# Optimization experiments

Hardware: AMD Instinct MI355X
Metric: run time of the kernel (lower is better)

Reference implementation:

```python
import jax, jax.numpy as jnp
import numpy as np

N, E, B, L, D, H = 50000, 800000, 64, 32, 256, 256


def setup_inputs() -> dict:
    key = jax.random.key(0)
    ks = jax.random.split(key, 20)
    s = 0.05
    inp = {
        'x': jax.random.normal(ks[0], (N, D), jnp.float32),
        'edge_index': jax.random.randint(ks[1], (2, E), 0, N),
        'batch': jnp.sort(jax.random.randint(ks[2], (N,), 0, B)),
        'paths': jax.random.randint(ks[3], (B, L), 0, N),
        # SAGEConv1: lin_l (aggregated neighbors, with bias) + lin_r (root, no bias)
        'w1l': jax.random.normal(ks[4], (D, H), jnp.float32) * s,
        'b1l': jnp.zeros((H,), jnp.float32),
        'w1r': jax.random.normal(ks[5], (D, H), jnp.float32) * s,
        # SAGEConv2
        'w2l': jax.random.normal(ks[6], (H, H), jnp.float32) * s,
        'b2l': jnp.zeros((H,), jnp.float32),
        'w2r': jax.random.normal(ks[7], (H, H), jnp.float32) * s,
        # LSTM (gate order i,f,g,o as in torch)
        'w_ih': jax.random.normal(ks[8], (4 * H, H), jnp.float32) * s,
        'w_hh': jax.random.normal(ks[9], (4 * H, H), jnp.float32) * s,
        'b_ih': jnp.zeros((4 * H,), jnp.float32),
        'b_hh': jnp.zeros((4 * H,), jnp.float32),
        # scorer MLP
        'wm1': jax.random.normal(ks[10], (2 * H, H), jnp.float32) * s,
        'bm1': jnp.zeros((H,), jnp.float32),
        'wm2': jax.random.normal(ks[11], (H, 1), jnp.float32) * s,
        'bm2': jnp.zeros((1,), jnp.float32),
    }
    return inp


def sage_conv(x, src, dst, wl, bl, wr):
    # mean-aggregate neighbor features (messages flow src -> dst)
    agg = jax.ops.segment_sum(x[src], dst, num_segments=N)
    deg = jax.ops.segment_sum(jnp.ones((src.shape[0],), x.dtype), dst, num_segments=N)
    mean = agg / jnp.maximum(deg, 1.0)[:, None]
    return mean @ wl + bl + x @ wr


def lstm_last_hidden(seq, w_ih, w_hh, b_ih, b_hh):
    # seq: [B, L, H] -> hn: [B, H]
    h0 = jnp.zeros((seq.shape[0], H), seq.dtype)
    c0 = jnp.zeros_like(h0)

    def step(carry, xt):
        h, c = carry
        gates = xt @ w_ih.T + b_ih + h @ w_hh.T + b_hh
        i, f, g, o = jnp.split(gates, 4, axis=-1)
        c = jax.nn.sigmoid(f) * c + jax.nn.sigmoid(i) * jnp.tanh(g)
        h = jax.nn.sigmoid(o) * jnp.tanh(c)
        return (h, c), None

    (hn, _), _ = jax.lax.scan(step, (h0, c0), jnp.swapaxes(seq, 0, 1))
    return hn


def reference(x, edge_index, batch, paths, w1l, b1l, w1r, w2l, b2l, w2r,
              w_ih, w_hh, b_ih, b_hh, wm1, bm1, wm2, bm2):
    src, dst = edge_index[0], edge_index[1]
    h = jax.nn.relu(sage_conv(x, src, dst, w1l, b1l, w1r))
    node_emb = sage_conv(h, src, dst, w2l, b2l, w2r)  # [N, H]

    # global mean pool per graph
    gsum = jax.ops.segment_sum(node_emb, batch, num_segments=B)
    gcnt = jax.ops.segment_sum(jnp.ones((N,), node_emb.dtype), batch, num_segments=B)
    graph_emb = gsum / jnp.maximum(gcnt, 1.0)[:, None]  # [B, H]

    path_seq = node_emb[paths]  # [B, L, H]
    path_emb = lstm_last_hidden(path_seq, w_ih, w_hh, b_ih, b_hh)  # [B, H]

    combined = jnp.concatenate([graph_emb, path_emb], axis=-1)  # [B, 2H]
    scores = jax.nn.relu(combined @ wm1 + bm1) @ wm2 + bm2  # [B, 1]
    return scores.reshape(-1)  # torch.cat of per-path [1] scores -> [B]
```

## Files before the change

### kernel.cpp

```cpp
#include <hip/hip_runtime.h>

namespace {

constexpr int NN = 50000;
constexpr int NE = 800000;
constexpr int NB = 64;
constexpr int NL = 32;
constexpr int ND = 256;
constexpr int NSCAN = 196;
constexpr int NPOOL = (NN + 63) / 64;

typedef __attribute__((ext_vector_type(8))) short short8v;
typedef __attribute__((ext_vector_type(4))) float float4v;

__device__ __forceinline__ float sigf(float x){ return 1.0f/(1.0f + __expf(-x)); }

__device__ __forceinline__ ushort rne_bf16(float f){
  uint u = __float_as_uint(f);
  return (ushort)((u + 0x7FFFu + ((u >> 16) & 1u)) >> 16);
}
__device__ __forceinline__ float bf2f(ushort u){ return __uint_as_float((uint)u << 16); }

__device__ __forceinline__ void splitr(float f, ushort& h, ushort& lo){
  h = rne_bf16(f);
  float r = f - bf2f(h);
  lo = (ushort)(__float_as_uint(r) >> 16);
}

__device__ __forceinline__ void split8(float4 fa, float4 fb, uint4& h, uint4& lo){
  uint a0=__float_as_uint(fa.x), a1=__float_as_uint(fa.y), a2=__float_as_uint(fa.z), a3=__float_as_uint(fa.w);
  uint b0=__float_as_uint(fb.x), b1=__float_as_uint(fb.y), b2=__float_as_uint(fb.z), b3=__float_as_uint(fb.w);
  h.x = (a0>>16) | (a1 & 0xFFFF0000u);
  h.y = (a2>>16) | (a3 & 0xFFFF0000u);
  h.z = (b0>>16) | (b1 & 0xFFFF0000u);
  h.w = (b2>>16) | (b3 & 0xFFFF0000u);
  float r0 = fa.x - __uint_as_float(a0 & 0xFFFF0000u);
  float r1 = fa.y - __uint_as_float(a1 & 0xFFFF0000u);
  float r2 = fa.z - __uint_as_float(a2 & 0xFFFF0000u);
  float r3 = fa.w - __uint_as_float(a3 & 0xFFFF0000u);
  float r4 = fb.x - __uint_as_float(b0 & 0xFFFF0000u);
  float r5 = fb.y - __uint_as_float(b1 & 0xFFFF0000u);
  float r6 = fb.z - __uint_as_float(b2 & 0xFFFF0000u);
  float r7 = fb.w - __uint_as_float(b3 & 0xFFFF0000u);
  lo.x = (__float_as_uint(r0)>>16) | (__float_as_uint(r1) & 0xFFFF0000u);
  lo.y = (__float_as_uint(r2)>>16) | (__float_as_uint(r3) & 0xFFFF0000u);
  lo.z = (__float_as_uint(r4)>>16) | (__float_as_uint(r5) & 0xFFFF0000u);
  lo.w = (__float_as_uint(r6)>>16) | (__float_as_uint(r7) & 0xFFFF0000u);
}

__global__ void k_hist(const int* __restrict__ dst, int* __restrict__ cnt){
  int stride = gridDim.x * blockDim.x;
  for (int e = blockIdx.x*blockDim.x + threadIdx.x; e < NE; e += stride)
    atomicAdd(&cnt[dst[e]], 1);
}

__global__ void k_scan_block(const int* __restrict__ cnt, int* __restrict__ offs,
                             int* __restrict__ bsum){
  __shared__ int s[256];
  const int t = threadIdx.x, i = blockIdx.x*256 + t;
  int v = cnt[i];
  s[t] = v; __syncthreads();
  #pragma unroll
  for (int off = 1; off < 256; off <<= 1){
    int x = (t >= off) ? s[t-off] : 0;
    __syncthreads();
    s[t] += x;
    __syncthreads();
  }
  offs[i] = s[t] - v;
  if (t == 255) bsum[blockIdx.x] = s[255];
}

__global__ void k_scan_top(const int* __restrict__ bsum, int* __restrict__ bsum2){
  __shared__ int s[256];
  const int t = threadIdx.x;
  int v = (t < NSCAN) ? bsum[t] : 0;
  s[t] = v; __syncthreads();
  #pragma unroll
  for (int off = 1; off < 256; off <<= 1){
    int x = (t >= off) ? s[t-off] : 0;
    __syncthreads();
    s[t] += x;
    __syncthreads();
  }
  if (t < NSCAN) bsum2[t] = s[t] - v;
}

__global__ void k_scan_add(int* __restrict__ offs, const int* __restrict__ bsum2,
                           int* __restrict__ cursor){
  const int i = blockIdx.x*256 + threadIdx.x;
  int v = offs[i] + bsum2[blockIdx.x];
  offs[i] = v;
  cursor[i] = v;
}

__global__ void k_fill(const int* __restrict__ src, const int* __restrict__ dst,
                       int* __restrict__ cursor, int* __restrict__ csr){
  int stride = gridDim.x * blockDim.x;
  for (int e = blockIdx.x*blockDim.x + threadIdx.x; e < NE; e += stride){
    int d = dst[e];
    int pos = atomicAdd(&cursor[d], 1);
    csr[pos] = src[e];
  }
}

__global__ void k_tobf16(const float* __restrict__ in, ushort* __restrict__ out){
  const int i = blockIdx.x*blockDim.x + threadIdx.x;
  const float4 a = ((const float4*)in)[i*2];
  const float4 b = ((const float4*)in)[i*2+1];
  ushort o[8] = { rne_bf16(a.x), rne_bf16(a.y), rne_bf16(a.z), rne_bf16(a.w),
                  rne_bf16(b.x), rne_bf16(b.y), rne_bf16(b.z), rne_bf16(b.w) };
  ((uint4*)out)[i] = *(uint4*)o;
}

__launch_bounds__(256, 8)
__global__ void k_gather_bf16(const ushort* __restrict__ feat, const int* __restrict__ offs,
                              const int* __restrict__ csr,
                              ushort* __restrict__ outH, ushort* __restrict__ outL){
  __shared__ float4 sp[256];
  const int u = blockIdx.x, t = threadIdx.x;
  const int w = t >> 6, l = t & 63;
  const int beg = offs[u], end = offs[u+1];
  const int lc = l * 4;
  float a0 = 0.f, a1 = 0.f, a2 = 0.f, a3 = 0.f;
  int e = beg + w;
  for (; e + 4 < end; e += 8){
    int s0 = csr[e], s1 = csr[e+4];
    ushort4 v0 = *(const ushort4*)(feat + (long long)s0*ND + lc);
    ushort4 v1 = *(const ushort4*)(feat + (long long)s1*ND + lc);
    a0 += bf2f(v0.x) + bf2f(v1.x);
    a1 += bf2f(v0.y) + bf2f(v1.y);
    a2 += bf2f(v0.z) + bf2f(v1.z);
    a3 += bf2f(v0.w) + bf2f(v1.w);
  }
  if (e < end){
    int s0 = csr[e];
    ushort4 v0 = *(const ushort4*)(feat + (long long)s0*ND + lc);
    a0 += bf2f(v0.x); a1 += bf2f(v0.y); a2 += bf2f(v0.z); a3 += bf2f(v0.w);
  }
  sp[t] = make_float4(a0, a1, a2, a3);
  __syncthreads();
  if (t < 64){
    float4 p0 = sp[t], p1 = sp[64+t], p2 = sp[128+t], p3 = sp[192+t];
    float inv = 1.0f / fmaxf((float)(end - beg), 1.0f);
    float4 r;
    r.x = (p0.x + p1.x + p2.x + p3.x) * inv;
    r.y = (p0.y + p1.y + p2.y + p3.y) * inv;
    r.z = (p0.z + p1.z + p2.z + p3.z) * inv;
    r.w = (p0.w + p1.w + p2.w + p3.w) * inv;
    ushort hh[4], ll[4];
    splitr(r.x, hh[0], ll[0]);
    splitr(r.y, hh[1], ll[1]);
    splitr(r.z, hh[2], ll[2]);
    splitr(r.w, hh[3], ll[3]);
    *(ushort4*)(outH + (long long)u*ND + t*4) = *(ushort4*)hh;
    *(ushort4*)(outL + (long long)u*ND + t*4) = *(ushort4*)ll;
  }
}

__global__ void k_wsplit(const float* __restrict__ wl, const float* __restrict__ wr,
                         ushort* __restrict__ WtH, ushort* __restrict__ WtL){
  const int k = blockIdx.x;
  const int n = threadIdx.x;
  float v = (k < 256) ? wl[k*256 + n] : wr[(k-256)*256 + n];
  uint u = __float_as_uint(v);
  float r = v - __uint_as_float(u & 0xFFFF0000u);
  const int wc = n >> 6, nt = (n >> 4) & 3, lm = n & 15;
  const int kk = k >> 5, lq = (k >> 3) & 3, j = k & 7;
  const long long idx = (long long)(((wc*4 + nt)*16 + kk)*64 + lq*16 + lm)*8 + j;
  WtH[idx] = (ushort)(u >> 16);
  WtL[idx] = (ushort)(__float_as_uint(r) >> 16);
}

template<int A2F32, int RELU>
__launch_bounds__(256, 2)
__global__ void k_gemm(const ushort* A1H, const ushort* A1L,
                       const ushort* A2H, const ushort* A2L,
                       const float*  A2F,
                       const ushort* __restrict__ WtH, const ushort* __restrict__ WtL,
                       const float* __restrict__ bias,
                       ushort* CH, ushort* CL)
{
  __shared__ float eb[16*260];
  const int t  = threadIdx.x;
  const int w  = t >> 6;
  const int l  = t & 63;
  const int lm = l & 15;
  const int lq = l >> 4;
  const int m0 = blockIdx.x * 64;

  const uint4* BH4 = (const uint4*)WtH;
  const uint4* BL4 = (const uint4*)WtL;

  const float4v vzero = {0.f, 0.f, 0.f, 0.f};
  float4v acc[4][4];
  #pragma unroll
  for (int i = 0; i < 4; ++i)
    #pragma unroll
    for (int j = 0; j < 4; ++j) acc[i][j] = vzero;

  long long arow[4];
  #pragma unroll
  for (int mt = 0; mt < 4; ++mt){
    int row = m0 + mt*16 + lm;
    row = (row < NN) ? row : (NN - 1);
    arow[mt] = (long long)row * ND;
  }
  int bbase[4];
  #pragma unroll
  for (int nt = 0; nt < 4; ++nt) bbase[nt] = (w*4 + nt)*1024 + l;

  uint4 aP[3][4], aQ[3][4];
  uint4 bh[2][4], bl[2][4];

  auto ldB = [&](int kk, int s){
    #pragma unroll
    for (int nt = 0; nt < 4; ++nt){
      const int idx = bbase[nt] + kk*64;
      bh[s][nt] = BH4[idx];
      bl[s][nt] = BL4[idx];
    }
  };
  auto ldA = [&](int kk, int s){
    const int koff = (kk & 7)*32 + lq*8;
    if (kk < 8 || !A2F32){
      const ushort* Hb = (kk < 8) ? A1H : A2H;
      const ushort* Lb = (kk < 8) ? A1L : A2L;
      #pragma unroll
      for (int mt = 0; mt < 4; ++mt){
        aP[s][mt] = *(const uint4*)(Hb + arow[mt] + koff);
        aQ[s][mt] = *(const uint4*)(Lb + arow[mt] + koff);
      }
    } else {
      #pragma unroll
      for (int mt = 0; mt < 4; ++mt){
        const float* p = A2F + arow[mt] + koff;
        aP[s][mt] = *(const uint4*)p;
        aQ[s][mt] = *(const uint4*)(p + 4);
      }
    }
  };

  ldA(0, 0);
  ldB(0, 0);
  ldA(1, 1);

  #pragma unroll
  for (int kk = 0; kk < 16; ++kk){
    const int c3 = kk % 3;
    const int cB = kk & 1;
    if (kk < 15) ldB(kk + 1, cB ^ 1);
    if (kk < 14) ldA(kk + 2, (kk + 2) % 3);
    __builtin_amdgcn_sched_barrier(0);

    uint4 ah[4], al[4];
    if (kk < 8 || !A2F32){
      #pragma unroll
      for (int mt = 0; mt < 4; ++mt){ ah[mt] = aP[c3][mt]; al[mt] = aQ[c3][mt]; }
    } else {
      #pragma unroll
      for (int mt = 0; mt < 4; ++mt){
        float4 fa = *(float4*)&aP[c3][mt];
        float4 fb = *(float4*)&aQ[c3][mt];
        split8(fa, fb, ah[mt], al[mt]);
      }
    }

    #pragma unroll
    for (int nt = 0; nt < 4; ++nt){
      short8v bhv = *(short8v*)&bh[cB][nt];
      short8v blv = *(short8v*)&bl[cB][nt];
      #pragma unroll
      for (int mt = 0; mt < 4; ++mt){
        short8v ahv = *(short8v*)&ah[mt];
        short8v alv = *(short8v*)&al[mt];
        acc[mt][nt] = __builtin_amdgcn_mfma_f32_16x16x32_bf16(ahv, bhv, acc[mt][nt], 0, 0, 0);
        acc[mt][nt] = __builtin_amdgcn_mfma_f32_16x16x32_bf16(alv, bhv, acc[mt][nt], 0, 0, 0);
        acc[mt][nt] = __builtin_amdgcn_mfma_f32_16x16x32_bf16(ahv, blv, acc[mt][nt], 0, 0, 0);
      }
    }
  }

  float bvv[4];
  #pragma unroll
  for (int nt = 0; nt < 4; ++nt) bvv[nt] = bias[w*64 + nt*16 + lm];

  #pragma unroll
  for (int mt = 0; mt < 4; ++mt){
    #pragma unroll
    for (int nt = 0; nt < 4; ++nt){
      #pragma unroll
      for (int r = 0; r < 4; ++r){
        float v = acc[mt][nt][r] + bvv[nt];
        if (RELU) v = fmaxf(v, 0.f);
        eb[(lq*4 + r)*260 + w*64 + nt*16 + lm] = v;
      }
    }
    __syncthreads();
    #pragma unroll
    for (int i = 0; i < 4; ++i){
      int idx = i*256 + t;
      int rr  = idx >> 6;
      int c4  = (idx & 63) * 4;
      int grow = m0 + mt*16 + rr;
      if (grow < NN){
        float4 fv = *(float4*)&eb[rr*260 + c4];
        ushort hh[4], ll[4];
        splitr(fv.x, hh[0], ll[0]);
        splitr(fv.y, hh[1], ll[1]);
        splitr(fv.z, hh[2], ll[2]);
        splitr(fv.w, hh[3], ll[3]);
        *(ushort4*)(CH + (long long)grow*ND + c4) = *(ushort4*)hh;
        *(ushort4*)(CL + (long long)grow*ND + c4) = *(ushort4*)ll;
      }
    }
    __syncthreads();
  }
}

__launch_bounds__(256, 3)
__global__ void k_xgate(const ushort* __restrict__ EH, const ushort* __restrict__ EL,
                        const int* __restrict__ paths,
                        const float* __restrict__ w_ih, const float* __restrict__ b_ih,
                        const float* __restrict__ b_hh, float* __restrict__ xg)
{
  __shared__ float As[16][68];
  __shared__ float Ws[16][260];
  const int t  = threadIdx.x;
  const int m0 = blockIdx.x * 64;
  const int g0 = blockIdx.y * 256;
  const int rg = t >> 5, cg = t & 31;
  const int sm = t >> 2, sj = (t & 3) * 4;

  float acc[8][8];
  #pragma unroll
  for (int i = 0; i < 8; ++i)
    #pragma unroll
    for (int j = 0; j < 8; ++j) acc[i][j] = 0.f;

  const int node = paths[m0 + sm];
  const ushort* ehrow = EH + (long long)node*ND;
  const ushort* elrow = EL + (long long)node*ND;
  const float* wrow = w_ih + (long long)(g0 + t)*ND;

  for (int k0 = 0; k0 < 256; k0 += 16){
    ushort4 hv = *(const ushort4*)(ehrow + k0 + sj);
    ushort4 lv = *(const ushort4*)(elrow + k0 + sj);
    float av0 = bf2f(hv.x) + bf2f(lv.x);
    float av1 = bf2f(hv.y) + bf2f(lv.y);
    float av2 = bf2f(hv.z) + bf2f(lv.z);
    float av3 = bf2f(hv.w) + bf2f(lv.w);
    float4 q0 = *(const float4*)(wrow + k0 + 0);
    float4 q1 = *(const float4*)(wrow + k0 + 4);
    float4 q2 = *(const float4*)(wrow + k0 + 8);
    float4 q3 = *(const float4*)(wrow + k0 + 12);
    __syncthreads();
    As[sj+0][sm]=av0; As[sj+1][sm]=av1; As[sj+2][sm]=av2; As[sj+3][sm]=av3;
    Ws[ 0][t]=q0.x; Ws[ 1][t]=q0.y; Ws[ 2][t]=q0.z; Ws[ 3][t]=q0.w;
    Ws[ 4][t]=q1.x; Ws[ 5][t]=q1.y; Ws[ 6][t]=q1.z; Ws[ 7][t]=q1.w;
    Ws[ 8][t]=q2.x; Ws[ 9][t]=q2.y; Ws[10][t]=q2.z; Ws[11][t]=q2.w;
    Ws[12][t]=q3.x; Ws[13][t]=q3.y; Ws[14][t]=q3.z; Ws[15][t]=q3.w;
    __syncthreads();
    #pragma unroll
    for (int k = 0; k < 16; ++k){
      float a[8], b[8];
      *(float4*)&a[0] = *(const float4*)&As[k][rg*8];
      *(float4*)&a[4] = *(const float4*)&As[k][rg*8+4];
      *(float4*)&b[0] = *(const float4*)&Ws[k][cg*8];
      *(float4*)&b[4] = *(const float4*)&Ws[k][cg*8+4];
      #pragma unroll
      for (int i = 0; i < 8; ++i)
        #pragma unroll
        for (int j = 0; j < 8; ++j)
          acc[i][j] = fmaf(a[i], b[j], acc[i][j]);
    }
  }

  float bv[8];
  #pragma unroll
  for (int j = 0; j < 8; ++j){ int g = g0 + cg*8 + j; bv[j] = b_ih[g] + b_hh[g]; }
  #pragma unroll
  for (int i = 0; i < 8; ++i){
    int row = m0 + rg*8 + i;
    float o[8];
    #pragma unroll
    for (int j = 0; j < 8; ++j) o[j] = acc[i][j] + bv[j];
    *(float4*)(xg + (long long)row*1024 + g0 + cg*8 + 0) = *(float4*)&o[0];
    *(float4*)(xg + (long long)row*1024 + g0 + cg*8 + 4) = *(float4*)&o[4];
  }
}

__launch_bounds__(256, 4)
__global__ void k_lstm_step(const float* __restrict__ h_in, float* __restrict__ h_out,
                            float* __restrict__ c_state, const float* __restrict__ xg,
                            const float* __restrict__ w_hh, int tstep)
{
  __shared__ float ws[4*256];
  __shared__ float hs[32*260];
  __shared__ float part[2*128];
  __shared__ float gs[128];
  const int t  = threadIdx.x;
  const int u  = blockIdx.x >> 1;
  const int b0 = (blockIdx.x & 1) * 32;

  {
    int gate = t >> 6, c4 = (t & 63) * 4;
    float4 v = *(const float4*)(w_hh + (long long)(gate*256 + u)*256 + c4);
    *(float4*)&ws[gate*256 + c4] = v;
  }
  #pragma unroll
  for (int i = 0; i < 8; ++i){
    int idx = i*256 + t;
    int b = idx >> 6, c4 = (idx & 63) * 4;
    float4 v = *(const float4*)(h_in + (long long)(b0 + b)*256 + c4);
    *(float4*)&hs[b*260 + c4] = v;
  }
  __syncthreads();

  const int b  = t & 31;
  const int g  = (t >> 5) & 3;
  const int kd = t >> 7;
  float s = 0.f;
  const float* hp = &hs[b*260 + kd*128];
  const float* wp = &ws[g*256 + kd*128];
  #pragma unroll
  for (int k4 = 0; k4 < 32; ++k4){
    float4 h4 = *(const float4*)(hp + k4*4);
    float4 w4 = *(const float4*)(wp + k4*4);
    s += h4.x*w4.x + h4.y*w4.y + h4.z*w4.z + h4.w*w4.w;
  }
  part[kd*128 + b*4 + g] = s;
  __syncthreads();

  if (t < 128){
    int bb = t >> 2, gg = t & 3;
    const float* xp = xg + ((long long)(b0 + bb)*NL + tstep)*1024;
    gs[t] = part[t] + part[128 + t] + xp[gg*256 + u];
  }
  __syncthreads();

  if (t < 32){
    float gi = gs[t*4+0], gf = gs[t*4+1], gG = gs[t*4+2], go = gs[t*4+3];
    int bb = b0 + t;
    float c_old = c_state[bb*256 + u];
    float c_new = sigf(gf)*c_old + sigf(gi)*tanhf(gG);
    c_state[bb*256 + u] = c_new;
    h_out[bb*256 + u] = sigf(go)*tanhf(c_new);
  }
}

__launch_bounds__(256, 8)
__global__ void k_pool(const ushort* __restrict__ EH, const ushort* __restrict__ EL,
                       const int* __restrict__ batch,
                       float* __restrict__ gsum, float* __restrict__ gcnt)
{
  __shared__ int bs[64];
  __shared__ int uni;
  __shared__ float spf[8*256];
  const int t  = threadIdx.x;
  const int m0 = blockIdx.x * 64;
  const int r  = t >> 5;
  const int c  = t & 31;
  if (t == 0) uni = 1;
  if (t < 64){
    int n = m0 + t;
    bs[t] = (n < NN) ? batch[n] : -1;
  }
  __syncthreads();
  if (t < 64 && bs[t] != bs[0]) uni = 0;
  __syncthreads();

  const ushort* eh = EH + (long long)m0*ND + c*8;
  const ushort* el = EL + (long long)m0*ND + c*8;

  if (uni){
    float a[8];
    #pragma unroll
    for (int j = 0; j < 8; ++j) a[j] = 0.f;
    #pragma unroll
    for (int i = 0; i < 8; ++i){
      const int row = r*8 + i;
      const uint4 hv = *(const uint4*)(eh + (long long)row*ND);
      const uint4 lv = *(const uint4*)(el + (long long)row*ND);
      const ushort* hp = (const ushort*)&hv;
      const ushort* lp = (const ushort*)&lv;
      #pragma unroll
      for (int j = 0; j < 8; ++j) a[j] += bf2f(hp[j]) + bf2f(lp[j]);
    }
    #pragma unroll
    for (int j = 0; j < 8; ++j) spf[r*256 + c*8 + j] = a[j];
    __syncthreads();
    float s = spf[t] + spf[256+t] + spf[512+t] + spf[768+t]
            + spf[1024+t] + spf[1280+t] + spf[1536+t] + spf[1792+t];
    const int g = bs[0];
    unsafeAtomicAdd(&gsum[g*256 + t], s);
    if (t == 0) unsafeAtomicAdd(&gcnt[g], 64.0f);
  } else {
    float a[8];
    #pragma unroll
    for (int j = 0; j < 8; ++j) a[j] = 0.f;
    int cur = -1, cnt = 0;
    #pragma unroll
    for (int i = 0; i < 8; ++i){
      const int row = r*8 + i;
      const int g = bs[row];
      if (g != cur){
        if (cur >= 0){
          #pragma unroll
          for (int j = 0; j < 8; ++j) unsafeAtomicAdd(&gsum[cur*256 + c*8 + j], a[j]);
          if (c == 0) unsafeAtomicAdd(&gcnt[cur], (float)cnt);
        }
        #pragma unroll
        for (int j = 0; j < 8; ++j) a[j] = 0.f;
        cnt = 0; cur = g;
      }
      if (g >= 0){
        const uint4 hv = *(const uint4*)(eh + (long long)row*ND);
        const uint4 lv = *(const uint4*)(el + (long long)row*ND);
        const ushort* hp = (const ushort*)&hv;
        const ushort* lp = (const ushort*)&lv;
        #pragma unroll
        for (int j = 0; j < 8; ++j) a[j] += bf2f(hp[j]) + bf2f(lp[j]);
        ++cnt;
      }
    }
    if (cur >= 0){
      #pragma unroll
      for (int j = 0; j < 8; ++j) unsafeAtomicAdd(&gsum[cur*256 + c*8 + j], a[j]);
      if (c == 0) unsafeAtomicAdd(&gcnt[cur], (float)cnt);
    }
  }
}

__global__ void k_score(const float* __restrict__ gsum, const float* __restrict__ gcnt,
                        const float* __restrict__ hfin, const float* __restrict__ wm1,
                        const float* __restrict__ bm1, const float* __restrict__ wm2,
                        const float* __restrict__ bm2, float* __restrict__ out)
{
  __shared__ float cs[512];
  __shared__ float red[4];
  const int b = blockIdx.x, t = threadIdx.x;
  float inv = 1.0f / fmaxf(gcnt[b], 1.0f);
  cs[t]       = gsum[b*256 + t] * inv;
  cs[256 + t] = hfin[b*256 + t];
  __syncthreads();
  float v = 0.f;
  #pragma unroll 4
  for (int k = 0; k < 512; ++k) v = fmaf(cs[k], wm1[(long long)k*256 + t], v);
  v = fmaxf(v + bm1[t], 0.f) * wm2[t];
  #pragma unroll
  for (int off = 32; off > 0; off >>= 1) v += __shfl_down(v, off, 64);
  if ((t & 63) == 0) red[t >> 6] = v;
  __syncthreads();
  if (t == 0) out[b] = red[0] + red[1] + red[2] + red[3] + bm2[0];
}

}

extern "C" void kernel_launch(void* const* d_in, const int* in_sizes, int n_in,
                              void* d_out, int out_size, void* d_ws, size_t ws_size,
                              hipStream_t stream)
{
  const float* x     = (const float*)d_in[0];
  const int*   eidx  = (const int*)  d_in[1];
  const int*   batch = (const int*)  d_in[2];
  const int*   paths = (const int*)  d_in[3];
  const float* w1l   = (const float*)d_in[4];
  const float* b1l   = (const float*)d_in[5];
  const float* w1r   = (const float*)d_in[6];
  const float* w2l   = (const float*)d_in[7];
  const float* b2l   = (const float*)d_in[8];
  const float* w2r   = (const float*)d_in[9];
  const float* w_ih  = (const float*)d_in[10];
  const float* w_hh  = (const float*)d_in[11];
  const float* b_ih  = (const float*)d_in[12];
  const float* b_hh  = (const float*)d_in[13];
  const float* wm1   = (const float*)d_in[14];
  const float* bm1   = (const float*)d_in[15];
  const float* wm2   = (const float*)d_in[16];
  const float* bm2   = (const float*)d_in[17];

  const int* src = eidx;
  const int* dst = eidx + NE;

  float* w    = (float*)d_ws;
  float* bufA = w;
  float* bufB = bufA + (long long)NN*ND;
  float* xg   = bufB + (long long)NN*ND;
  float* gsum = xg   + 2048*1024;
  float* gcnt = gsum + NB*ND;
  float* h0   = gcnt + 64;
  float* c0   = h0   + NB*ND;
  float* h1   = c0   + NB*ND;
  ushort* wt1H = (ushort*)(h1 + NB*ND);
  ushort* wt1L = wt1H + 256*512;
  ushort* wt2H = wt1L + 256*512;
  ushort* wt2L = wt2H + 256*512;
  ushort* fb16 = wt2L + 256*512;

  ushort* A1H = (ushort*)bufA;
  ushort* A1L = A1H + (long long)NN*ND;
  ushort* h1H = (ushort*)bufB;
  ushort* h1L = h1H + (long long)NN*ND;

  int* cnt    = (int*)xg;
  int* offs   = cnt    + 50432;
  int* cursor = offs   + 50432;
  int* bsum   = cursor + 50432;
  int* bsum2  = bsum   + 256;
  int* csr    = bsum2  + 256;

  k_wsplit<<<512, 256, 0, stream>>>(w1l, w1r, wt1H, wt1L);
  k_wsplit<<<512, 256, 0, stream>>>(w2l, w2r, wt2H, wt2L);

  k_tobf16<<<(NN*ND/8 + 255)/256, 256, 0, stream>>>(x, fb16);

  hipMemsetAsync(cnt, 0, 50432*sizeof(int), stream);
  k_hist<<<1024, 256, 0, stream>>>(dst, cnt);
  k_scan_block<<<NSCAN, 256, 0, stream>>>(cnt, offs, bsum);
  k_scan_top<<<1, 256, 0, stream>>>(bsum, bsum2);
  k_scan_add<<<NSCAN, 256, 0, stream>>>(offs, bsum2, cursor);
  k_fill<<<1024, 256, 0, stream>>>(src, dst, cursor, csr);

  k_gather_bf16<<<NN, 256, 0, stream>>>(fb16, offs, csr, A1H, A1L);
  k_gemm<1,1><<<782, 256, 0, stream>>>(A1H, A1L, nullptr, nullptr, x,
                                       wt1H, wt1L, b1l, h1H, h1L);

  k_gather_bf16<<<NN, 256, 0, stream>>>(h1H, offs, csr, A1H, A1L);
  k_gemm<0,0><<<782, 256, 0, stream>>>(A1H, A1L, h1H, h1L, nullptr,
                                       wt2H, wt2L, b2l, h1H, h1L);

  hipMemsetAsync(gsum, 0, (NB*ND + 64)*sizeof(float), stream);
  k_pool<<<NPOOL, 256, 0, stream>>>(h1H, h1L, batch, gsum, gcnt);

  k_xgate<<<dim3((NB*NL)/64, 1024/256), 256, 0, stream>>>(h1H, h1L, paths, w_ih, b_ih, b_hh, xg);

  hipMemsetAsync(h0, 0, 2*(size_t)NB*ND*sizeof(float), stream);
  for (int ts = 0; ts < NL; ++ts){
    float* hin  = (ts & 1) ? h1 : h0;
    float* hout = (ts & 1) ? h0 : h1;
    k_lstm_step<<<512, 256, 0, stream>>>(hin, hout, c0, xg, w_hh, ts);
  }

  k_score<<<NB, 256, 0, stream>>>(gsum, gcnt, h0, wm1, bm1, wm2, bm2, (float*)d_out);
}
```

Baseline: 816.6 us.

## Fuse per-timestep LSTM launches into one persistent per-batch kernel

Replaces 32 per-timestep LSTM kernel launches with a single kernel where each block owns one batch row and iterates all timesteps, keeping h in shared memory and c in registers. This removes launch overhead and global round trips of hidden/cell state between steps. In exchange, only 64 blocks run and every block streams the full w_hh from cache each step, which reduces parallelism and increases L2 traffic.

New measurement: 1.713 ms. 110% more time.

```diff
diff --git a/kernel.cpp b/kernel.cpp
--- a/kernel.cpp
+++ b/kernel.cpp
@@ -390,62 +390,49 @@
   }
 }
 
-__launch_bounds__(256, 4)
-__global__ void k_lstm_step(const float* __restrict__ h_in, float* __restrict__ h_out,
-                            float* __restrict__ c_state, const float* __restrict__ xg,
-                            const float* __restrict__ w_hh, int tstep)
+__launch_bounds__(1024, 4)
+__global__ void k_lstm_batch(const float* __restrict__ xg, const float* __restrict__ w_hh,
+                             float* __restrict__ hfin)
 {
-  __shared__ float ws[4*256];
-  __shared__ float hs[32*260];
-  __shared__ float part[2*128];
-  __shared__ float gs[128];
-  const int t  = threadIdx.x;
-  const int u  = blockIdx.x >> 1;
-  const int b0 = (blockIdx.x & 1) * 32;
-
-  {
-    int gate = t >> 6, c4 = (t & 63) * 4;
-    float4 v = *(const float4*)(w_hh + (long long)(gate*256 + u)*256 + c4);
-    *(float4*)&ws[gate*256 + c4] = v;
-  }
-  #pragma unroll
-  for (int i = 0; i < 8; ++i){
-    int idx = i*256 + t;
-    int b = idx >> 6, c4 = (idx & 63) * 4;
-    float4 v = *(const float4*)(h_in + (long long)(b0 + b)*256 + c4);
-    *(float4*)&hs[b*260 + c4] = v;
-  }
-  __syncthreads();
-
-  const int b  = t & 31;
-  const int g  = (t >> 5) & 3;
-  const int kd = t >> 7;
-  float s = 0.f;
-  const float* hp = &hs[b*260 + kd*128];
-  const float* wp = &ws[g*256 + kd*128];
-  #pragma unroll
-  for (int k4 = 0; k4 < 32; ++k4){
-    float4 h4 = *(const float4*)(hp + k4*4);
-    float4 w4 = *(const float4*)(wp + k4*4);
-    s += h4.x*w4.x + h4.y*w4.y + h4.z*w4.z + h4.w*w4.w;
-  }
-  part[kd*128 + b*4 + g] = s;
-  __syncthreads();
-
-  if (t < 128){
-    int bb = t >> 2, gg = t & 3;
-    const float* xp = xg + ((long long)(b0 + bb)*NL + tstep)*1024;
-    gs[t] = part[t] + part[128 + t] + xp[gg*256 + u];
-  }
-  __syncthreads();
-
-  if (t < 32){
-    float gi = gs[t*4+0], gf = gs[t*4+1], gG = gs[t*4+2], go = gs[t*4+3];
-    int bb = b0 + t;
-    float c_old = c_state[bb*256 + u];
-    float c_new = sigf(gf)*c_old + sigf(gi)*tanhf(gG);
-    c_state[bb*256 + u] = c_new;
-    h_out[bb*256 + u] = sigf(go)*tanhf(c_new);
+  __shared__ float hcur[256];
+  __shared__ float gs[1024];
+  const int t = threadIdx.x;
+  const int b = blockIdx.x;
+  const float* wrow = w_hh + (long long)t * 256;
+  float c_reg = 0.f;
+
+  for (int ts = 0; ts < NL; ++ts){
+    float s;
+    if (ts == 0){
+      s = 0.f;
+    } else {
+      float s0 = 0.f, s1 = 0.f;
+      #pragma unroll
+      for (int k4 = 0; k4 < 32; ++k4){
+        float4 h4 = *(const float4*)&hcur[k4*4];
+        float4 w4 = *(const float4*)(wrow + k4*4);
+        s0 += h4.x*w4.x + h4.y*w4.y + h4.z*w4.z + h4.w*w4.w;
+      }
+      #pragma unroll
+      for (int k4 = 32; k4 < 64; ++k4){
+        float4 h4 = *(const float4*)&hcur[k4*4];
+        float4 w4 = *(const float4*)(wrow + k4*4);
+        s1 += h4.x*w4.x + h4.y*w4.y + h4.z*w4.z + h4.w*w4.w;
+      }
+      s = s0 + s1;
+    }
+    s += xg[((long long)b*NL + ts)*1024 + t];
+    gs[t] = s;
+    __syncthreads();
+    if (t < 256){
+      float gi = gs[t], gf = gs[256+t], gG = gs[512+t], go = gs[768+t];
+      float c_new = sigf(gf)*c_reg + sigf(gi)*tanhf(gG);
+      c_reg = c_new;
+      float h = sigf(go)*tanhf(c_new);
+      hcur[t] = h;
+      if (ts == NL-1) hfin[b*256 + t] = h;
+    }
+    __syncthreads();
   }
 }
 
@@ -635,12 +622,7 @@
 
   k_xgate<<<dim3((NB*NL)/64, 1024/256), 256, 0, stream>>>(h1H, h1L, paths, w_ih, b_ih, b_hh, xg);
 
-  hipMemsetAsync(h0, 0, 2*(size_t)NB*ND*sizeof(float), stream);
-  for (int ts = 0; ts < NL; ++ts){
-    float* hin  = (ts & 1) ? h1 : h0;
-    float* hout = (ts & 1) ? h0 : h1;
-    k_lstm_step<<<512, 256, 0, stream>>>(hin, hout, c0, xg, w_hh, ts);
-  }
+  k_lstm_batch<<<NB, 1024, 0, stream>>>(xg, w_hh, h0);
 
   k_score<<<NB, 256, 0, stream>>>(gsum, gcnt, h0, wm1, bm1, wm2, bm2, (float*)d_out);
 }
```
